# Kernel optimization log

Measured on AMD Instinct MI355X. Metric: run time of the kernel, lower is better.

## Reference

```python
import jax, jax.numpy as jnp
import numpy as np

RADIUS = 1.0
NORM_ORD = 2.0
N_POINTS = 4194304


def _contract(p):
    # p: [..., 3] -> contracted points [..., 3] (MipNeRF-360 eq. 10)
    eps = jnp.finfo(p.dtype).eps
    mag = jnp.linalg.norm(p, ord=NORM_ORD, axis=-1)
    mag = jnp.maximum(mag, eps)
    norm_factor = (2.0 - RADIUS / mag) / mag
    mask = (mag <= RADIUS)[..., None]
    return jnp.where(mask, p / RADIUS, norm_factor[..., None] * p)


def setup_inputs() -> dict:
    key = jax.random.key(0)
    x = jax.random.normal(key, (N_POINTS, 3), dtype=jnp.float32) * 2.0
    return {"x": x, "output_jacobian": 1}


def reference(x, output_jacobian):
    x_contr = _contract(x)
    if output_jacobian:
        # per-point 3x3 jacobian, mirroring torch.func.vmap(jacrev(contract))
        jacobian = jax.vmap(jax.jacrev(_contract))(x.reshape(-1, x.shape[-1]))
        jacobian = jacobian.reshape(x.shape[:-1] + (x.shape[-1], x.shape[-1]))
        return (x_contr, jacobian)
    return x_contr
```

## Files before the change

kernel.cpp:

```cpp
#include <hip/hip_runtime.h>


__global__ __launch_bounds__(256) void contract_jac_kernel(
    const float* __restrict__ x,
    float* __restrict__ out,
    int n_groups,
    long long n_points)
{
    int t = blockIdx.x * blockDim.x + threadIdx.x;
    if (t >= n_groups) return;

    const float4* xv = reinterpret_cast<const float4*>(x) + (size_t)t * 3;
    float4 v0 = xv[0];
    float4 v1 = xv[1];
    float4 v2 = xv[2];

    float p[4][3] = {
        {v0.x, v0.y, v0.z},
        {v0.w, v1.x, v1.y},
        {v1.z, v1.w, v2.x},
        {v2.y, v2.z, v2.w},
    };

    float oc[12];
    float oj[36];

    #pragma unroll
    for (int k = 0; k < 4; ++k) {
        float px = p[k][0], py = p[k][1], pz = p[k][2];
        float m2 = fmaf(px, px, fmaf(py, py, pz * pz));
        float m  = sqrtf(m2);

        float s, coef;
        if (m <= 1.0f) {
            s = 1.0f;
            coef = 0.0f;
        } else {
            float inv = 1.0f / m;
            s = (2.0f - inv) * inv;
            coef = 2.0f * (1.0f - m) / (m2 * m2);
        }

        oc[k*3+0] = s * px;
        oc[k*3+1] = s * py;
        oc[k*3+2] = s * pz;

        float cx = coef * px;
        float cy = coef * py;
        float cz = coef * pz;
        oj[k*9+0] = fmaf(cx, px, s);
        oj[k*9+1] = cx * py;
        oj[k*9+2] = cx * pz;
        oj[k*9+3] = cy * px;
        oj[k*9+4] = fmaf(cy, py, s);
        oj[k*9+5] = cy * pz;
        oj[k*9+6] = cz * px;
        oj[k*9+7] = cz * py;
        oj[k*9+8] = fmaf(cz, pz, s);
    }

    float4* oc4 = reinterpret_cast<float4*>(out) + (size_t)t * 3;
    #pragma unroll
    for (int i = 0; i < 3; ++i)
        oc4[i] = make_float4(oc[i*4+0], oc[i*4+1], oc[i*4+2], oc[i*4+3]);

    float4* oj4 = reinterpret_cast<float4*>(out + (size_t)n_points * 3) + (size_t)t * 9;
    #pragma unroll
    for (int i = 0; i < 9; ++i)
        oj4[i] = make_float4(oj[i*4+0], oj[i*4+1], oj[i*4+2], oj[i*4+3]);
}

extern "C" void kernel_launch(void* const* d_in, const int* in_sizes, int n_in,
                              void* d_out, int out_size, void* d_ws, size_t ws_size,
                              hipStream_t stream) {
    const float* x = (const float*)d_in[0];
    float* out = (float*)d_out;

    long long n = in_sizes[0] / 3;
    int groups = (int)(n / 4);
    int block = 256;
    int grid = (groups + block - 1) / block;

    contract_jac_kernel<<<grid, block, 0, stream>>>(x, out, groups, n);
}
```

Measured before the change: 264.2 us.

## Stage inputs and outputs through shared memory for fully coalesced float4 accesses

Each block now cooperatively loads 1024 points into LDS with contiguous float4 loads, and each thread processes four strided points. Results are written back to LDS and then streamed out with coalesced float4 stores, for both the contracted points and the Jacobians. The goal is to replace the per-thread strided 48B/144B vector accesses with fully contiguous wavefront transactions. In exchange it adds 36KB of LDS per block, several barriers and LDS bank conflicts from the stride-3 and stride-9 accesses. It also drops the tail bound check, so it assumes N is a multiple of 1024.

Result: faster. 239.3 us (-9.4%).

```diff
diff --git a/kernel.cpp b/kernel.cpp
--- a/kernel.cpp
+++ b/kernel.cpp
@@ -1,33 +1,34 @@
 #include <hip/hip_runtime.h>
 
 
-__global__ __launch_bounds__(256) void contract_jac_kernel(
+constexpr int BLOCK = 256;
+constexpr int PPB   = 1024;
+
+__global__ __launch_bounds__(BLOCK) void contract_jac_kernel(
     const float* __restrict__ x,
     float* __restrict__ out,
-    int n_groups,
     long long n_points)
 {
-    int t = blockIdx.x * blockDim.x + threadIdx.x;
-    if (t >= n_groups) return;
+    __shared__ float4 sbuf[PPB * 9 / 4];
 
-    const float4* xv = reinterpret_cast<const float4*>(x) + (size_t)t * 3;
-    float4 v0 = xv[0];
-    float4 v1 = xv[1];
-    float4 v2 = xv[2];
+    const int tid = threadIdx.x;
+    float* sw = reinterpret_cast<float*>(sbuf);
 
-    float p[4][3] = {
-        {v0.x, v0.y, v0.z},
-        {v0.w, v1.x, v1.y},
-        {v1.z, v1.w, v2.x},
-        {v2.y, v2.z, v2.w},
-    };
+    const float4* x4 = reinterpret_cast<const float4*>(x) + (long long)blockIdx.x * 768;
+    #pragma unroll
+    for (int i = 0; i < 3; ++i)
+        sbuf[tid + i * BLOCK] = x4[tid + i * BLOCK];
+    __syncthreads();
 
     float oc[12];
     float oj[36];
-
     #pragma unroll
     for (int k = 0; k < 4; ++k) {
-        float px = p[k][0], py = p[k][1], pz = p[k][2];
+        const int j = tid + k * BLOCK;
+        float px = sw[j * 3 + 0];
+        float py = sw[j * 3 + 1];
+        float pz = sw[j * 3 + 2];
+
         float m2 = fmaf(px, px, fmaf(py, py, pz * pz));
         float m  = sqrtf(m2);
 
@@ -41,33 +42,49 @@
             coef = 2.0f * (1.0f - m) / (m2 * m2);
         }
 
-        oc[k*3+0] = s * px;
-        oc[k*3+1] = s * py;
-        oc[k*3+2] = s * pz;
+        oc[k * 3 + 0] = s * px;
+        oc[k * 3 + 1] = s * py;
+        oc[k * 3 + 2] = s * pz;
 
-        float cx = coef * px;
-        float cy = coef * py;
-        float cz = coef * pz;
-        oj[k*9+0] = fmaf(cx, px, s);
-        oj[k*9+1] = cx * py;
-        oj[k*9+2] = cx * pz;
-        oj[k*9+3] = cy * px;
-        oj[k*9+4] = fmaf(cy, py, s);
-        oj[k*9+5] = cy * pz;
-        oj[k*9+6] = cz * px;
-        oj[k*9+7] = cz * py;
-        oj[k*9+8] = fmaf(cz, pz, s);
+        float cx = coef * px, cy = coef * py, cz = coef * pz;
+        oj[k * 9 + 0] = fmaf(cx, px, s);
+        oj[k * 9 + 1] = cx * py;
+        oj[k * 9 + 2] = cx * pz;
+        oj[k * 9 + 3] = cy * px;
+        oj[k * 9 + 4] = fmaf(cy, py, s);
+        oj[k * 9 + 5] = cy * pz;
+        oj[k * 9 + 6] = cz * px;
+        oj[k * 9 + 7] = cz * py;
+        oj[k * 9 + 8] = fmaf(cz, pz, s);
     }
+    __syncthreads();
 
-    float4* oc4 = reinterpret_cast<float4*>(out) + (size_t)t * 3;
+    #pragma unroll
+    for (int k = 0; k < 4; ++k) {
+        const int j = tid + k * BLOCK;
+        sw[j * 3 + 0] = oc[k * 3 + 0];
+        sw[j * 3 + 1] = oc[k * 3 + 1];
+        sw[j * 3 + 2] = oc[k * 3 + 2];
+    }
+    __syncthreads();
+    float4* oc4 = reinterpret_cast<float4*>(out) + (long long)blockIdx.x * 768;
     #pragma unroll
     for (int i = 0; i < 3; ++i)
-        oc4[i] = make_float4(oc[i*4+0], oc[i*4+1], oc[i*4+2], oc[i*4+3]);
+        oc4[tid + i * BLOCK] = sbuf[tid + i * BLOCK];
+    __syncthreads();
 
-    float4* oj4 = reinterpret_cast<float4*>(out + (size_t)n_points * 3) + (size_t)t * 9;
+    #pragma unroll
+    for (int k = 0; k < 4; ++k) {
+        const int j = tid + k * BLOCK;
+        #pragma unroll
+        for (int c = 0; c < 9; ++c)
+            sw[j * 9 + c] = oj[k * 9 + c];
+    }
+    __syncthreads();
+    float4* oj4 = reinterpret_cast<float4*>(out + n_points * 3) + (long long)blockIdx.x * 2304;
     #pragma unroll
     for (int i = 0; i < 9; ++i)
-        oj4[i] = make_float4(oj[i*4+0], oj[i*4+1], oj[i*4+2], oj[i*4+3]);
+        oj4[tid + i * BLOCK] = sbuf[tid + i * BLOCK];
 }
 
 extern "C" void kernel_launch(void* const* d_in, const int* in_sizes, int n_in,
@@ -77,9 +94,7 @@
     float* out = (float*)d_out;
 
     long long n = in_sizes[0] / 3;
-    int groups = (int)(n / 4);
-    int block = 256;
-    int grid = (groups + block - 1) / block;
+    int grid = (int)(n / PPB);
 
-    contract_jac_kernel<<<grid, block, 0, stream>>>(x, out, groups, n);
+    contract_jac_kernel<<<grid, BLOCK, 0, stream>>>(x, out, n);
 }
```
